# Optimization experiments

Measured on AMD Instinct MI355X. Metric: run time of the kernel, lower is better.

## Reference

```python
import jax, jax.numpy as jnp
import numpy as np

G = 32            # group_dim
N = 2             # feature batch (becomes 3N after repeat)
H = 192
W = 192
C_EXTRA = 32      # channels of the extra input tensor
POOLING_SIZE = (5, 9, 17)
POOLING_CHAN = (1, 1, 1)  # scaled by group_dim inside the module


def conv1x1(x, w, b):
    # x: [B, Cin, H, W], w: [Cout, Cin], b: [Cout]
    return jnp.einsum('bchw,oc->bohw', x, w) + b[None, :, None, None]


def integral_image(x):
    # x: [B, C, H, W] -> summed-area table [B, C, H+1, W+1] with zero top row / left col
    s = jnp.cumsum(jnp.cumsum(x, axis=2), axis=3)
    return jnp.pad(s, ((0, 0), (0, 0), (1, 0), (1, 0)))


def box_sums(S, half, h, w):
    # S: [B, C, h+1, w+1]; returns per-pixel box sums [B, C, h, w] and area [h, w]
    y = jnp.arange(h)
    x = jnp.arange(w)
    y0 = jnp.maximum(y - half, 0)
    y1 = jnp.minimum(y + 1 + half, h)
    x0 = jnp.maximum(x - half, 0)
    x1 = jnp.minimum(x + 1 + half, w)
    Sy0 = S[:, :, y0, :]
    Sy1 = S[:, :, y1, :]
    s = Sy1[:, :, :, x1] - Sy1[:, :, :, x0] - Sy0[:, :, :, x1] + Sy0[:, :, :, x0]
    area = ((y1 - y0)[:, None] * (x1 - x0)[None, :]).astype(S.dtype)
    return s, area


def setup_inputs() -> dict:
    key = jax.random.key(0)
    ks = jax.random.split(key, 10)
    C = G + C_EXTRA  # channels after concat with image_ctx
    c1_out = (G + 2) // 2 * 4
    inp = {
        'feature': jax.random.normal(ks[0], (N, G, H, W), jnp.float32),
        'extra': jax.random.normal(ks[1], (3 * N, C_EXTRA, H, W), jnp.float32),
        'w_ctx': jax.random.normal(ks[2], (G, G), jnp.float32) * 0.05,
        'b_ctx': jnp.zeros((G,), jnp.float32),
        'w1': jax.random.normal(ks[3], (c1_out, C), jnp.float32) * 0.05,
        'b1': jnp.zeros((c1_out,), jnp.float32),
    }
    for i in range(3):
        oc = 2 * G * POOLING_CHAN[i]
        inp['w_s%d' % i] = jax.random.normal(ks[4 + i], (oc, 2 * C), jnp.float32) * 0.05
        inp['b_s%d' % i] = jnp.zeros((oc,), jnp.float32)
    return inp


def reference(feature, extra, w_ctx, b_ctx, w1, b1,
              w_s0, b_s0, w_s1, b_s1, w_s2, b_s2):
    img_ctx = conv1x1(feature, w_ctx, b_ctx)          # [N, G, H, W]
    img_ctx = jnp.repeat(img_ctx, 3, axis=0)          # [3N, G, H, W]
    x = jnp.concatenate([img_ctx, extra], axis=1)     # [3N, C, H, W]
    _, _, h, w = x.shape

    outs = [conv1x1(x, w1, b1)]

    S1 = integral_image(x)
    S2 = integral_image(x * x)

    scale_params = ((w_s0, b_s0), (w_s1, b_s1), (w_s2, b_s2))
    for ps, (ws, bs) in zip(POOLING_SIZE, scale_params):
        half = ps // 2
        s1, area = box_sums(S1, half, h, w)
        s2, _ = box_sums(S2, half, h, w)
        mean = s1 / area
        var = s2 / area - mean * mean
        outs.append(conv1x1(jnp.concatenate([mean, var], axis=1), ws, bs))

    return jnp.concatenate(outs, axis=1)  # [3N, 68 + 3*64 = 260, H, W]
```

## Files before the change

kernel.cpp:

```cpp
#include <hip/hip_runtime.h>

#define H 192
#define W 192
#define HW (H*W)
#define G 32
#define C 64
#define C2 128
#define C1 68
#define B 6
#define NB 2
#define OUTC 260
#define STRIP 48

__global__ __launch_bounds__(256) void ctx_kernel(
    const float* __restrict__ feature, const float* __restrict__ w_ctx,
    const float* __restrict__ b_ctx, float* __restrict__ ctx)
{
    int p = blockIdx.x * 256 + threadIdx.x;
    int b = blockIdx.y;
    float f[G];
    const float* fp = feature + (size_t)b * G * HW + p;
#pragma unroll
    for (int k = 0; k < G; k++) f[k] = fp[k * HW];
    float* op = ctx + (size_t)b * G * HW + p;
    for (int o = 0; o < G; o++) {
        float acc = b_ctx[o];
#pragma unroll
        for (int k = 0; k < G; k++) acc += w_ctx[o * G + k] * f[k];
        op[o * HW] = acc;
    }
}

__global__ __launch_bounds__(256) void conv1_kernel(
    const float* __restrict__ ctx, const float* __restrict__ extra,
    const float* __restrict__ w1, const float* __restrict__ b1,
    float* __restrict__ out)
{
    int p = blockIdx.x * 256 + threadIdx.x;
    int b = blockIdx.y;
    float xv[C];
    const float* cp = ctx + (size_t)(b / 3) * G * HW + p;
#pragma unroll
    for (int k = 0; k < G; k++) xv[k] = cp[k * HW];
    const float* ep = extra + (size_t)b * G * HW + p;
#pragma unroll
    for (int k = 0; k < G; k++) xv[G + k] = ep[k * HW];
    float* op = out + (size_t)b * OUTC * HW + p;
    for (int o = 0; o < C1; o++) {
        float acc = b1[o];
#pragma unroll
        for (int k = 0; k < C; k++) acc += w1[o * C + k] * xv[k];
        op[o * HW] = acc;
    }
}

__global__ __launch_bounds__(256) void transpose_w_kernel(
    const float* __restrict__ wsrc, float* __restrict__ wT, int oc, int ic)
{
    int i = blockIdx.x * 256 + threadIdx.x;
    if (i >= oc * ic) return;
    int o = i / ic, c = i % ic;
    wT[c * oc + o] = wsrc[i];
}

__global__ __launch_bounds__(192) void mv_kernel(
    const float* __restrict__ ctx, const float* __restrict__ extra,
    int half, int bbase, float* __restrict__ mv)
{
    __shared__ float ls1[2][W];
    __shared__ float ls2[2][W];
    int w = threadIdx.x;
    int c = blockIdx.x;
    int s = blockIdx.y;
    int bz = blockIdx.z;
    int b = bbase + bz;
    const float* src = (c < G)
        ? (ctx + ((size_t)(b / 3) * G + c) * HW)
        : (extra + ((size_t)b * G + (c - G)) * HW);

    int h0 = s * STRIP;
    int ya = max(h0 - half, 0);
    int yb = min(h0 + half, H - 1);
    float s1 = 0.f, s2 = 0.f;
    for (int y = ya; y <= yb; y++) { float v = src[y * W + w]; s1 += v; s2 += v * v; }

    int x0 = max(w - half, 0);
    int x1 = min(w + half, W - 1);
    float ncols = (float)(x1 - x0 + 1);

    size_t obase = ((size_t)bz * C2 + c) * HW;

    for (int h = h0; h < h0 + STRIP; h++) {
        if (h > h0) {
            int yadd = h + half;
            int ysub = h - half - 1;
            if (yadd <= H - 1) { float v = src[yadd * W + w]; s1 += v; s2 += v * v; }
            if (ysub >= 0)     { float v = src[ysub * W + w]; s1 -= v; s2 -= v * v; }
        }
        int buf = h & 1;
        ls1[buf][w] = s1;
        ls2[buf][w] = s2;
        __syncthreads();
        float t1 = 0.f, t2 = 0.f;
        for (int x = x0; x <= x1; x++) { t1 += ls1[buf][x]; t2 += ls2[buf][x]; }
        int nrows = min(h + half, H - 1) - max(h - half, 0) + 1;
        float inv_area = 1.0f / ((float)nrows * ncols);
        float mean = t1 * inv_area;
        float var  = t2 * inv_area - mean * mean;
        mv[obase + h * W + w] = mean;
        mv[obase + (size_t)C * HW + h * W + w] = var;
    }
}

__global__ __launch_bounds__(256) void sconv_kernel(
    const float* __restrict__ mv, const float* __restrict__ wT,
    const float* __restrict__ bsc, int bbase, int co, float* __restrict__ out)
{
    int p = blockIdx.x * 256 + threadIdx.x;
    int bz = blockIdx.y;
    int b = bbase + bz;
    const float* xp = mv + (size_t)bz * C2 * HW + p;
    float acc[C];
#pragma unroll
    for (int o = 0; o < C; o++) acc[o] = 0.f;
#pragma unroll 2
    for (int c = 0; c < C2; c++) {
        float v = xp[(size_t)c * HW];
        const float* wrow = wT + c * C;
#pragma unroll
        for (int o = 0; o < C; o++) acc[o] += wrow[o] * v;
    }
    float* op = out + ((size_t)b * OUTC + co) * HW + p;
#pragma unroll
    for (int o = 0; o < C; o++) op[o * HW] = acc[o] + bsc[o];
}

extern "C" void kernel_launch(void* const* d_in, const int* in_sizes, int n_in,
                              void* d_out, int out_size, void* d_ws, size_t ws_size,
                              hipStream_t stream) {
    const float* feature = (const float*)d_in[0];
    const float* extra   = (const float*)d_in[1];
    const float* w_ctx   = (const float*)d_in[2];
    const float* b_ctx   = (const float*)d_in[3];
    const float* w1      = (const float*)d_in[4];
    const float* b1      = (const float*)d_in[5];
    const float* w_s[3]  = {(const float*)d_in[6], (const float*)d_in[8], (const float*)d_in[10]};
    const float* b_s[3]  = {(const float*)d_in[7], (const float*)d_in[9], (const float*)d_in[11]};
    float* out = (float*)d_out;

    float* ctx = (float*)d_ws;
    float* wT  = ctx + (size_t)NB * G * HW;
    float* mv  = wT + 3 * C2 * C;

    size_t base_bytes = ((size_t)NB * G * HW + 3 * C2 * C) * 4;
    size_t mv_full = (size_t)B * C2 * HW * 4;
    bool batched = ws_size >= base_bytes + mv_full;

    ctx_kernel<<<dim3(HW / 256, NB), 256, 0, stream>>>(feature, w_ctx, b_ctx, ctx);
    conv1_kernel<<<dim3(HW / 256, B), 256, 0, stream>>>(ctx, extra, w1, b1, out);

    for (int si = 0; si < 3; si++) {
        transpose_w_kernel<<<dim3((C2 * C + 255) / 256), 256, 0, stream>>>(
            w_s[si], wT + si * C2 * C, C, C2);
    }

    const int halves[3] = {2, 4, 8};
    if (batched) {
        for (int si = 0; si < 3; si++) {
            mv_kernel<<<dim3(C, H / STRIP, B), W, 0, stream>>>(ctx, extra, halves[si], 0, mv);
            sconv_kernel<<<dim3(HW / 256, B), 256, 0, stream>>>(
                mv, wT + si * C2 * C, b_s[si], 0, C1 + si * C, out);
        }
    } else {
        for (int si = 0; si < 3; si++) {
            for (int b = 0; b < B; b++) {
                mv_kernel<<<dim3(C, H / STRIP, 1), W, 0, stream>>>(ctx, extra, halves[si], b, mv);
                sconv_kernel<<<dim3(HW / 256, 1), 256, 0, stream>>>(
                    mv, wT + si * C2 * C, b_s[si], b, C1 + si * C, out);
            }
        }
    }
}
```

Baseline: 718.5 us.

## Fuse all three box-filter scales into one mean/var pass with DPP prefix scans

Replaces the three per-scale mean/var passes with one kernel that keeps running column sums for all three window sizes. It computes the horizontal box sums from a wave-level DPP inclusive scan plus a cross-wave offset, instead of a serial loop over up to 17 shared-memory entries. Mean and variance are stored interleaved as float2, and one 3D-grid conv kernel handles all scales against weights transposed to match that layout. This cuts launches, repeated reads of the input channels and redundant horizontal summation. In exchange it needs a larger workspace for all three scales' intermediates, and the prefix-difference form may lose a little floating-point precision.

```diff
diff --git a/kernel.cpp b/kernel.cpp
--- a/kernel.cpp
+++ b/kernel.cpp
@@ -11,6 +11,8 @@
 #define NB 2
 #define OUTC 260
 #define STRIP 48
+#define STRIP_R 48
+
 
 __global__ __launch_bounds__(256) void ctx_kernel(
     const float* __restrict__ feature, const float* __restrict__ w_ctx,
@@ -53,6 +55,155 @@
         op[o * HW] = acc;
     }
 }
+
+
+template<int CTRL, int RM>
+__device__ __forceinline__ float dpp_mov0(float x) {
+    return __int_as_float(__builtin_amdgcn_update_dpp(
+        0, __float_as_int(x), CTRL, RM, 0xf, false));
+}
+__device__ __forceinline__ float wave_iscan(float x) {
+    x += dpp_mov0<0x111, 0xf>(x);
+    x += dpp_mov0<0x112, 0xf>(x);
+    x += dpp_mov0<0x114, 0xf>(x);
+    x += dpp_mov0<0x118, 0xf>(x);
+    x += dpp_mov0<0x142, 0xa>(x);
+    x += dpp_mov0<0x143, 0xc>(x);
+    return x;
+}
+
+__global__ __launch_bounds__(256) void transpose_wi_kernel(
+    const float* __restrict__ w0, const float* __restrict__ w1,
+    const float* __restrict__ w2, float* __restrict__ wTi)
+{
+    int i = blockIdx.x * 256 + threadIdx.x;
+    if (i >= 3 * C * C2) return;
+    int si = i / (C * C2);
+    int r = i % (C * C2);
+    const float* ws = (si == 0) ? w0 : (si == 1) ? w1 : w2;
+    int o = r / C2, ci = r % C2;
+    int dst = (ci < C) ? (ci * (2 * C) + o) : ((ci - C) * (2 * C) + C + o);
+    wTi[si * (C2 * C) + dst] = ws[r];
+}
+
+__global__ __launch_bounds__(192) void mv_all_kernel(
+    const float* __restrict__ ctx, const float* __restrict__ extra,
+    int bbase, int nbs, float* __restrict__ mv)
+{
+    __shared__ float2 pls[2][3][W];
+    __shared__ float2 wsum[2][3][3];
+    const int hk0 = 2, hk1 = 4, hk2 = 8;
+    const int hks[3] = {hk0, hk1, hk2};
+
+    int w = threadIdx.x;
+    int lane = w & 63;
+    int wv = w >> 6;
+    int c = blockIdx.x;
+    int bz = blockIdx.z;
+    int b = bbase + bz;
+    const float* src = (c < G) ? (ctx + ((size_t)(b / 3) * G + c) * HW)
+                               : (extra + ((size_t)b * G + (c - G)) * HW);
+    int h0 = blockIdx.y * STRIP_R;
+
+    float s1[3] = {0.f, 0.f, 0.f}, s2[3] = {0.f, 0.f, 0.f};
+#pragma unroll
+    for (int dy = -hk2; dy <= hk2; ++dy) {
+        int y = h0 + dy;
+        float v = (y >= 0 && y < H) ? src[y * W + w] : 0.f;
+        float vv = v * v;
+        if (dy >= -hk0 && dy <= hk0) { s1[0] += v; s2[0] += vv; }
+        if (dy >= -hk1 && dy <= hk1) { s1[1] += v; s2[1] += vv; }
+        s1[2] += v; s2[2] += vv;
+    }
+
+    float inv_nc[3];
+    int x1i[3], x0m[3];
+#pragma unroll
+    for (int k = 0; k < 3; ++k) {
+        int x0 = max(w - hks[k], 0), x1 = min(w + hks[k], W - 1);
+        x1i[k] = x1;
+        x0m[k] = w - hks[k] - 1;
+        inv_nc[k] = 1.0f / (float)(x1 - x0 + 1);
+    }
+    size_t sstride = (size_t)nbs * C * HW;
+    float2* mvp = (float2*)mv + ((size_t)bz * C + c) * HW;
+
+    for (int h = h0; h < h0 + STRIP_R; ++h) {
+        if (h > h0) {
+#pragma unroll
+            for (int k = 0; k < 3; ++k) {
+                int ya = h + hks[k], ys = h - hks[k] - 1;
+                if (ya < H)  { float v = src[ya * W + w]; s1[k] += v; s2[k] = fmaf(v, v, s2[k]); }
+                if (ys >= 0) { float v = src[ys * W + w]; s1[k] -= v; s2[k] = fmaf(-v, v, s2[k]); }
+            }
+        }
+        int buf = h & 1;
+        float p1[3], p2[3];
+#pragma unroll
+        for (int k = 0; k < 3; ++k) { p1[k] = wave_iscan(s1[k]); p2[k] = wave_iscan(s2[k]); }
+        if (lane == 63) {
+#pragma unroll
+            for (int k = 0; k < 3; ++k) wsum[buf][k][wv] = make_float2(p1[k], p2[k]);
+        }
+        __syncthreads();
+#pragma unroll
+        for (int k = 0; k < 3; ++k) {
+            float2 w0v = wsum[buf][k][0];
+            float2 w1v = wsum[buf][k][1];
+            float o1 = 0.f, o2 = 0.f;
+            if (wv >= 1) { o1 += w0v.x; o2 += w0v.y; }
+            if (wv >= 2) { o1 += w1v.x; o2 += w1v.y; }
+            pls[buf][k][w] = make_float2(p1[k] + o1, p2[k] + o2);
+        }
+        __syncthreads();
+#pragma unroll
+        for (int k = 0; k < 3; ++k) {
+            float2 hi = pls[buf][k][x1i[k]];
+            int xm = x0m[k];
+            float2 lo = pls[buf][k][xm < 0 ? 0 : xm];
+            if (xm < 0) { lo.x = 0.f; lo.y = 0.f; }
+            float t1 = hi.x - lo.x;
+            float t2 = hi.y - lo.y;
+            float inv_nr;
+            if (h >= hks[k] && h + hks[k] < H) inv_nr = 1.0f / (float)(2 * hks[k] + 1);
+            else inv_nr = 1.0f / (float)(min(h + hks[k], H - 1) - max(h - hks[k], 0) + 1);
+            float ia = inv_nr * inv_nc[k];
+            float mean = t1 * ia;
+            float var = fmaf(t2, ia, -(mean * mean));
+            mvp[(size_t)k * sstride + h * W + w] = make_float2(mean, var);
+        }
+    }
+}
+
+__global__ __launch_bounds__(256) void sconv_all_kernel(
+    const float* __restrict__ mv, const float* __restrict__ wTi,
+    const float* __restrict__ bs0, const float* __restrict__ bs1,
+    const float* __restrict__ bs2,
+    int bbase, int nbs, float* __restrict__ out)
+{
+    int p = blockIdx.x * 256 + threadIdx.x;
+    int bz = blockIdx.y;
+    int si = blockIdx.z;
+    size_t sstride = (size_t)nbs * C * HW;
+    const float2* xp = (const float2*)mv + (size_t)si * sstride + (size_t)bz * C * HW + p;
+    const float* wp = wTi + si * (C2 * C);
+    float acc[C];
+#pragma unroll
+    for (int o = 0; o < C; ++o) acc[o] = 0.f;
+#pragma unroll 2
+    for (int c = 0; c < C; ++c) {
+        float2 v = xp[(size_t)c * HW];
+        const float* wrow = wp + c * (2 * C);
+#pragma unroll
+        for (int o = 0; o < C; ++o)
+            acc[o] = fmaf(wrow[o], v.x, fmaf(wrow[C + o], v.y, acc[o]));
+    }
+    const float* bs = (si == 0) ? bs0 : (si == 1) ? bs1 : bs2;
+    float* op = out + ((size_t)(bbase + bz) * OUTC + C1 + si * C) * HW + p;
+#pragma unroll
+    for (int o = 0; o < C; ++o) op[o * HW] = acc[o] + bs[o];
+}
+
 
 __global__ __launch_bounds__(256) void transpose_w_kernel(
     const float* __restrict__ wsrc, float* __restrict__ wT, int oc, int ic)
@@ -135,6 +286,7 @@
     for (int o = 0; o < C; o++) op[o * HW] = acc[o] + bsc[o];
 }
 
+
 extern "C" void kernel_launch(void* const* d_in, const int* in_sizes, int n_in,
                               void* d_out, int out_size, void* d_ws, size_t ws_size,
                               hipStream_t stream) {
@@ -153,31 +305,40 @@
     float* mv  = wT + 3 * C2 * C;
 
     size_t base_bytes = ((size_t)NB * G * HW + 3 * C2 * C) * 4;
+    size_t mv_new = (size_t)B * 3 * C * HW * 2 * 4;
     size_t mv_full = (size_t)B * C2 * HW * 4;
-    bool batched = ws_size >= base_bytes + mv_full;
+    bool newpath = ws_size >= base_bytes + mv_new;
 
     ctx_kernel<<<dim3(HW / 256, NB), 256, 0, stream>>>(feature, w_ctx, b_ctx, ctx);
     conv1_kernel<<<dim3(HW / 256, B), 256, 0, stream>>>(ctx, extra, w1, b1, out);
 
-    for (int si = 0; si < 3; si++) {
-        transpose_w_kernel<<<dim3((C2 * C + 255) / 256), 256, 0, stream>>>(
-            w_s[si], wT + si * C2 * C, C, C2);
-    }
-
-    const int halves[3] = {2, 4, 8};
-    if (batched) {
-        for (int si = 0; si < 3; si++) {
-            mv_kernel<<<dim3(C, H / STRIP, B), W, 0, stream>>>(ctx, extra, halves[si], 0, mv);
-            sconv_kernel<<<dim3(HW / 256, B), 256, 0, stream>>>(
-                mv, wT + si * C2 * C, b_s[si], 0, C1 + si * C, out);
-        }
+    if (newpath) {
+        transpose_wi_kernel<<<dim3((3 * C * C2 + 255) / 256), 256, 0, stream>>>(
+            w_s[0], w_s[1], w_s[2], wT);
+        mv_all_kernel<<<dim3(C, H / STRIP_R, B), W, 0, stream>>>(ctx, extra, 0, B, mv);
+        sconv_all_kernel<<<dim3(HW / 256, B, 3), 256, 0, stream>>>(
+            mv, wT, b_s[0], b_s[1], b_s[2], 0, B, out);
     } else {
         for (int si = 0; si < 3; si++) {
-            for (int b = 0; b < B; b++) {
-                mv_kernel<<<dim3(C, H / STRIP, 1), W, 0, stream>>>(ctx, extra, halves[si], b, mv);
-                sconv_kernel<<<dim3(HW / 256, 1), 256, 0, stream>>>(
-                    mv, wT + si * C2 * C, b_s[si], b, C1 + si * C, out);
+            transpose_w_kernel<<<dim3((C2 * C + 255) / 256), 256, 0, stream>>>(
+                w_s[si], wT + si * C2 * C, C, C2);
+        }
+        const int halves[3] = {2, 4, 8};
+        bool batched = ws_size >= base_bytes + mv_full;
+        if (batched) {
+            for (int si = 0; si < 3; si++) {
+                mv_kernel<<<dim3(C, H / STRIP, B), W, 0, stream>>>(ctx, extra, halves[si], 0, mv);
+                sconv_kernel<<<dim3(HW / 256, B), 256, 0, stream>>>(
+                    mv, wT + si * C2 * C, b_s[si], 0, C1 + si * C, out);
             }
-        }
-    }
-}
+        } else {
+            for (int si = 0; si < 3; si++) {
+                for (int b = 0; b < B; b++) {
+                    mv_kernel<<<dim3(C, H / STRIP, 1), W, 0, stream>>>(ctx, extra, halves[si], b, mv);
+                    sconv_kernel<<<dim3(HW / 256, 1), 256, 0, stream>>>(
+                        mv, wT + si * C2 * C, b_s[si], b, C1 + si * C, out);
+                }
+            }
+        }
+    }
+}
```

Result: no change. 705.4 us (-1.8%).

## Fuse box-filter mean/var with scale 1x1 conv in one tiled kernel

Applied to the files above, without the earlier changes.

Replaces the separate mean/variance kernel and the per-scale 1x1 conv with one fused kernel per (column tile, row strip, batch×scale). Each block keeps vertical running sums in registers, does the horizontal box sums with a DPP wave prefix scan, stages mean/var and weights in LDS, and computes the 64-output conv with register tiling. This removes the large mv intermediate round-trip through global memory and several launches. In exchange it recomputes halo columns (48 useful of 64 lanes) and uses many registers per thread.

```diff
diff --git a/kernel.cpp b/kernel.cpp
--- a/kernel.cpp
+++ b/kernel.cpp
@@ -10,7 +10,8 @@
 #define B 6
 #define NB 2
 #define OUTC 260
-#define STRIP 48
+#define RSTRIP 24
+
 
 __global__ __launch_bounds__(256) void ctx_kernel(
     const float* __restrict__ feature, const float* __restrict__ w_ctx,
@@ -54,86 +55,167 @@
     }
 }
 
-__global__ __launch_bounds__(256) void transpose_w_kernel(
-    const float* __restrict__ wsrc, float* __restrict__ wT, int oc, int ic)
+__global__ __launch_bounds__(256) void transpose_wi_kernel(
+    const float* __restrict__ w0, const float* __restrict__ w1,
+    const float* __restrict__ w2, float* __restrict__ wTi)
 {
     int i = blockIdx.x * 256 + threadIdx.x;
-    if (i >= oc * ic) return;
-    int o = i / ic, c = i % ic;
-    wT[c * oc + o] = wsrc[i];
-}
-
-__global__ __launch_bounds__(192) void mv_kernel(
+    if (i >= 3 * C * C2) return;
+    int si = i / (C * C2);
+    int r = i % (C * C2);
+    const float* ws = (si == 0) ? w0 : (si == 1) ? w1 : w2;
+    int o = r / C2, ci = r % C2;
+    int dst = (ci < C) ? (ci * (2 * C) + o) : ((ci - C) * (2 * C) + C + o);
+    wTi[si * (C2 * C) + dst] = ws[r];
+}
+
+
+template<int CTRL, int RM>
+__device__ __forceinline__ float dpp_mov0(float x) {
+    return __int_as_float(__builtin_amdgcn_update_dpp(
+        0, __float_as_int(x), CTRL, RM, 0xf, false));
+}
+__device__ __forceinline__ float wave_iscan(float x) {
+    x += dpp_mov0<0x111, 0xf>(x);
+    x += dpp_mov0<0x112, 0xf>(x);
+    x += dpp_mov0<0x114, 0xf>(x);
+    x += dpp_mov0<0x118, 0xf>(x);
+    x += dpp_mov0<0x142, 0xa>(x);
+    x += dpp_mov0<0x143, 0xc>(x);
+    return x;
+}
+
+__global__ __launch_bounds__(192) void fused_mv_sconv_kernel(
     const float* __restrict__ ctx, const float* __restrict__ extra,
-    int half, int bbase, float* __restrict__ mv)
-{
-    __shared__ float ls1[2][W];
-    __shared__ float ls2[2][W];
-    int w = threadIdx.x;
-    int c = blockIdx.x;
-    int s = blockIdx.y;
-    int bz = blockIdx.z;
-    int b = bbase + bz;
-    const float* src = (c < G)
-        ? (ctx + ((size_t)(b / 3) * G + c) * HW)
-        : (extra + ((size_t)b * G + (c - G)) * HW);
-
-    int h0 = s * STRIP;
-    int ya = max(h0 - half, 0);
-    int yb = min(h0 + half, H - 1);
-    float s1 = 0.f, s2 = 0.f;
-    for (int y = ya; y <= yb; y++) { float v = src[y * W + w]; s1 += v; s2 += v * v; }
-
-    int x0 = max(w - half, 0);
-    int x1 = min(w + half, W - 1);
-    float ncols = (float)(x1 - x0 + 1);
-
-    size_t obase = ((size_t)bz * C2 + c) * HW;
-
-    for (int h = h0; h < h0 + STRIP; h++) {
+    const float* __restrict__ wTi,
+    const float* __restrict__ bs0, const float* __restrict__ bs1,
+    const float* __restrict__ bs2, float* __restrict__ out)
+{
+    __shared__ __align__(16) float ls_w[C][2][C];
+    __shared__ __align__(16) float ls_mv[C][2][48];
+    __shared__ float ls_b[C];
+
+    int t = threadIdx.x;
+    int wv = t >> 6, lane = t & 63;
+    int sx = blockIdx.x, sy = blockIdx.y;
+    int b = blockIdx.z / 3, si = blockIdx.z % 3;
+    int hk = (si == 0) ? 2 : (si == 1) ? 4 : 8;
+
+    const float* wp = wTi + si * (C2 * C);
+    for (int i = t; i < C * C2; i += 192)
+        ls_w[i >> 7][(i >> 6) & 1][i & 63] = wp[i];
+    const float* bsp = (si == 0) ? bs0 : (si == 1) ? bs1 : bs2;
+    if (t < C) ls_b[t] = bsp[t];
+
+    int col = sx * 48 - 8 + lane;
+    bool colok = (col >= 0) && (col < W);
+    bool outok = (lane >= 8) && (lane < 56);
+    int h0 = sy * RSTRIP;
+
+    const float* cbase = ctx + (size_t)(b / 3) * G * HW;
+    const float* ebase = extra + ((size_t)b * G - G) * HW;
+
+    float s1[22], s2[22];
+#pragma unroll
+    for (int j = 0; j < 22; ++j) {
+        int c = wv + 3 * j;
+        if (c < C) {
+            const float* src = ((c < G) ? cbase : ebase) + (size_t)c * HW;
+            float a1 = 0.f, a2 = 0.f;
+            for (int y = h0 - hk; y <= h0 + hk; ++y) {
+                if (colok && y >= 0 && y < H) {
+                    float v = src[y * W + col];
+                    a1 += v; a2 = fmaf(v, v, a2);
+                }
+            }
+            s1[j] = a1; s2[j] = a2;
+        }
+    }
+
+    float inv_nc;
+    {
+        int x0 = max(col - hk, 0), x1 = min(col + hk, W - 1);
+        inv_nc = 1.0f / (float)(x1 - x0 + 1);
+    }
+    float inv_full = 1.0f / (float)(2 * hk + 1);
+
+    int pxg = t % 12, og = t / 12;
+
+    for (int h = h0; h < h0 + RSTRIP; ++h) {
         if (h > h0) {
-            int yadd = h + half;
-            int ysub = h - half - 1;
-            if (yadd <= H - 1) { float v = src[yadd * W + w]; s1 += v; s2 += v * v; }
-            if (ysub >= 0)     { float v = src[ysub * W + w]; s1 -= v; s2 -= v * v; }
-        }
-        int buf = h & 1;
-        ls1[buf][w] = s1;
-        ls2[buf][w] = s2;
+            int ya = h + hk, ys = h - hk - 1;
+            bool la = (ya < H), lsub = (ys >= 0);
+#pragma unroll
+            for (int j = 0; j < 22; ++j) {
+                int c = wv + 3 * j;
+                if (c < C) {
+                    const float* src = ((c < G) ? cbase : ebase) + (size_t)c * HW;
+                    if (colok) {
+                        if (la)   { float v = src[ya * W + col]; s1[j] += v; s2[j] = fmaf(v, v, s2[j]); }
+                        if (lsub) { float v = src[ys * W + col]; s1[j] -= v; s2[j] = fmaf(-v, v, s2[j]); }
+                    }
+                }
+            }
+        }
+        float inv_nr = (h >= hk && h + hk < H) ? inv_full
+                     : 1.0f / (float)(min(h + hk, H - 1) - max(h - hk, 0) + 1);
+        float ia = inv_nr * inv_nc;
+#pragma unroll
+        for (int j = 0; j < 22; ++j) {
+            int c = wv + 3 * j;
+            if (c < C) {
+                float p1 = wave_iscan(s1[j]);
+                float p2 = wave_iscan(s2[j]);
+                int ihi = lane + hk;
+                int ilo = lane - hk - 1;
+                float h1 = __shfl(p1, ihi & 63);
+                float h2 = __shfl(p2, ihi & 63);
+                float l1 = __shfl(p1, ilo & 63);
+                float l2 = __shfl(p2, ilo & 63);
+                if (ilo < 0) { l1 = 0.f; l2 = 0.f; }
+                if (outok) {
+                    float mean = (h1 - l1) * ia;
+                    float var  = fmaf(h2 - l2, ia, -(mean * mean));
+                    ls_mv[c][0][lane - 8] = mean;
+                    ls_mv[c][1][lane - 8] = var;
+                }
+            }
+        }
         __syncthreads();
-        float t1 = 0.f, t2 = 0.f;
-        for (int x = x0; x <= x1; x++) { t1 += ls1[buf][x]; t2 += ls2[buf][x]; }
-        int nrows = min(h + half, H - 1) - max(h - half, 0) + 1;
-        float inv_area = 1.0f / ((float)nrows * ncols);
-        float mean = t1 * inv_area;
-        float var  = t2 * inv_area - mean * mean;
-        mv[obase + h * W + w] = mean;
-        mv[obase + (size_t)C * HW + h * W + w] = var;
-    }
-}
-
-__global__ __launch_bounds__(256) void sconv_kernel(
-    const float* __restrict__ mv, const float* __restrict__ wT,
-    const float* __restrict__ bsc, int bbase, int co, float* __restrict__ out)
-{
-    int p = blockIdx.x * 256 + threadIdx.x;
-    int bz = blockIdx.y;
-    int b = bbase + bz;
-    const float* xp = mv + (size_t)bz * C2 * HW + p;
-    float acc[C];
-#pragma unroll
-    for (int o = 0; o < C; o++) acc[o] = 0.f;
+
+        float acc[16];
+#pragma unroll
+        for (int i = 0; i < 16; ++i) acc[i] = 0.f;
 #pragma unroll 2
-    for (int c = 0; c < C2; c++) {
-        float v = xp[(size_t)c * HW];
-        const float* wrow = wT + c * C;
-#pragma unroll
-        for (int o = 0; o < C; o++) acc[o] += wrow[o] * v;
-    }
-    float* op = out + ((size_t)b * OUTC + co) * HW + p;
-#pragma unroll
-    for (int o = 0; o < C; o++) op[o * HW] = acc[o] + bsc[o];
-}
+        for (int c = 0; c < C; ++c) {
+            float4 m4  = *(const float4*)&ls_mv[c][0][pxg * 4];
+            float4 v4  = *(const float4*)&ls_mv[c][1][pxg * 4];
+            float4 wm4 = *(const float4*)&ls_w[c][0][og * 4];
+            float4 wv4 = *(const float4*)&ls_w[c][1][og * 4];
+            float m_[4] = {m4.x, m4.y, m4.z, m4.w};
+            float v_[4] = {v4.x, v4.y, v4.z, v4.w};
+            float wm_[4] = {wm4.x, wm4.y, wm4.z, wm4.w};
+            float wv_[4] = {wv4.x, wv4.y, wv4.z, wv4.w};
+#pragma unroll
+            for (int px = 0; px < 4; ++px)
+#pragma unroll
+                for (int o = 0; o < 4; ++o)
+                    acc[px * 4 + o] = fmaf(wm_[o], m_[px],
+                                      fmaf(wv_[o], v_[px], acc[px * 4 + o]));
+        }
+        float* op = out + ((size_t)b * OUTC + C1 + si * C + og * 4) * HW
+                  + h * W + sx * 48 + pxg * 4;
+#pragma unroll
+        for (int o = 0; o < 4; ++o) {
+            float bb = ls_b[og * 4 + o];
+            *(float4*)(op + (size_t)o * HW) = make_float4(
+                acc[0 * 4 + o] + bb, acc[1 * 4 + o] + bb,
+                acc[2 * 4 + o] + bb, acc[3 * 4 + o] + bb);
+        }
+        __syncthreads();
+    }
+}
+
 
 extern "C" void kernel_launch(void* const* d_in, const int* in_sizes, int n_in,
                               void* d_out, int out_size, void* d_ws, size_t ws_size,
@@ -150,34 +232,11 @@
 
     float* ctx = (float*)d_ws;
     float* wT  = ctx + (size_t)NB * G * HW;
-    float* mv  = wT + 3 * C2 * C;
-
-    size_t base_bytes = ((size_t)NB * G * HW + 3 * C2 * C) * 4;
-    size_t mv_full = (size_t)B * C2 * HW * 4;
-    bool batched = ws_size >= base_bytes + mv_full;
 
     ctx_kernel<<<dim3(HW / 256, NB), 256, 0, stream>>>(feature, w_ctx, b_ctx, ctx);
+    transpose_wi_kernel<<<dim3((3 * C * C2 + 255) / 256), 256, 0, stream>>>(
+        w_s[0], w_s[1], w_s[2], wT);
     conv1_kernel<<<dim3(HW / 256, B), 256, 0, stream>>>(ctx, extra, w1, b1, out);
-
-    for (int si = 0; si < 3; si++) {
-        transpose_w_kernel<<<dim3((C2 * C + 255) / 256), 256, 0, stream>>>(
-            w_s[si], wT + si * C2 * C, C, C2);
-    }
-
-    const int halves[3] = {2, 4, 8};
-    if (batched) {
-        for (int si = 0; si < 3; si++) {
-            mv_kernel<<<dim3(C, H / STRIP, B), W, 0, stream>>>(ctx, extra, halves[si], 0, mv);
-            sconv_kernel<<<dim3(HW / 256, B), 256, 0, stream>>>(
-                mv, wT + si * C2 * C, b_s[si], 0, C1 + si * C, out);
-        }
-    } else {
-        for (int si = 0; si < 3; si++) {
-            for (int b = 0; b < B; b++) {
-                mv_kernel<<<dim3(C, H / STRIP, 1), W, 0, stream>>>(ctx, extra, halves[si], b, mv);
-                sconv_kernel<<<dim3(HW / 256, 1), 256, 0, stream>>>(
-                    mv, wT + si * C2 * C, b_s[si], b, C1 + si * C, out);
-            }
-        }
-    }
-}
+    fused_mv_sconv_kernel<<<dim3(W / 48, H / RSTRIP, 3 * B), 192, 0, stream>>>(
+        ctx, extra, wT, b_s[0], b_s[1], b_s[2], out);
+}
```

New measurement: 1.280 ms. 78.2% more time.
